# Performance work log

Hardware: AMD Instinct MI355X
Metric: run time of the kernel (lower is better)

## Reference

```python
import jax, jax.numpy as jnp
import numpy as np

EPS = 1e-5  # torch InstanceNorm2d default eps


def setup_inputs() -> dict:
    key = jax.random.key(0)
    k1, k2, k3, k4 = jax.random.split(key, 4)
    B, C, H, W = 32, 256, 64, 64
    S = 16
    x = jax.random.normal(k1, (B, C, H, W), dtype=jnp.float32)
    style_id = jax.random.randint(k2, (B,), 0, S, dtype=jnp.int64)
    gamma = jax.random.normal(k3, (S, C), dtype=jnp.float32)
    beta = jax.random.normal(k4, (S, C), dtype=jnp.float32)
    return {"x": x, "style_id": style_id, "gamma": gamma, "beta": beta}


def reference(x, style_id, gamma, beta):
    # Per-sample, per-channel instance norm over spatial dims (biased var),
    # with style-indexed affine params (torch InstanceNorm2d, affine=True).
    mean = jnp.mean(x, axis=(2, 3), keepdims=True)          # [B,C,1,1]
    var = jnp.mean(jnp.square(x - mean), axis=(2, 3), keepdims=True)
    x_hat = (x - mean) * jax.lax.rsqrt(var + EPS)
    g = gamma[style_id][:, :, None, None]                   # [B,C,1,1]
    b = beta[style_id][:, :, None, None]
    return x_hat * g + b
```

## Files before the change

kernel.cpp:

```cpp
#include <hip/hip_runtime.h>


#define HW   4096
#define NC   256
#define NTHR 256

typedef float vfloat4 __attribute__((ext_vector_type(4)));

__global__ __launch_bounds__(NTHR) void cin2d_kernel(
    const float* __restrict__ x,
    const int* __restrict__ style_id,
    const float* __restrict__ gamma,
    const float* __restrict__ beta,
    float* __restrict__ out)
{
    const int wave = threadIdx.x >> 6;
    const int lane = threadIdx.x & 63;
    const int inst = (blockIdx.x << 2) + wave;
    const int b = inst >> 8;
    const int c = inst & (NC - 1);

    const vfloat4* xp = (const vfloat4*)(x + (size_t)inst * HW) + lane;

    vfloat4 d[16];
#pragma unroll
    for (int i = 0; i < 16; ++i) d[i] = __builtin_nontemporal_load(xp + i * 64);

#pragma unroll
    for (int i = 0; i < 16; ++i) asm volatile("" : "+v"(d[i]));

    const int sid = style_id[b];
    const float g  = gamma[sid * NC + c];
    const float be = beta[sid * NC + c];

    float s0 = 0.f, s1 = 0.f, s2 = 0.f, s3 = 0.f;
    float q0 = 0.f, q1 = 0.f, q2 = 0.f, q3 = 0.f;
#pragma unroll
    for (int i = 0; i < 16; ++i) {
        s0 += d[i][0];  q0 = fmaf(d[i][0], d[i][0], q0);
        s1 += d[i][1];  q1 = fmaf(d[i][1], d[i][1], q1);
        s2 += d[i][2];  q2 = fmaf(d[i][2], d[i][2], q2);
        s3 += d[i][3];  q3 = fmaf(d[i][3], d[i][3], q3);
    }
    float s = (s0 + s1) + (s2 + s3);
    float q = (q0 + q1) + (q2 + q3);

#pragma unroll
    for (int off = 1; off < 64; off <<= 1) {
        s += __shfl_xor(s, off, 64);
        q += __shfl_xor(q, off, 64);
    }

    const float inv_n = 1.0f / (float)HW;
    const float mean = s * inv_n;
    float var = fmaf(-mean, mean, q * inv_n);
    var = var < 0.0f ? 0.0f : var;
    const float rstd = rsqrtf(var + 1e-5f);

    const float scale = g * rstd;
    const float shift = fmaf(-mean, scale, be);

    vfloat4* op = (vfloat4*)(out + (size_t)inst * HW) + lane;
#pragma unroll
    for (int i = 0; i < 16; ++i) {
        vfloat4 w;
#pragma unroll
        for (int j = 0; j < 4; ++j) w[j] = fmaf(d[i][j], scale, shift);
        op[i * 64] = w;
    }
}

extern "C" void kernel_launch(void* const* d_in, const int* in_sizes, int n_in,
                              void* d_out, int out_size, void* d_ws, size_t ws_size,
                              hipStream_t stream) {
    const float* x     = (const float*)d_in[0];
    const int*   sid   = (const int*)d_in[1];
    const float* gamma = (const float*)d_in[2];
    const float* beta  = (const float*)d_in[3];
    float* out = (float*)d_out;

    const int B = 32, C = 256;
    dim3 grid((B * C) / 4), block(NTHR);
    hipLaunchKernelGGL(cin2d_kernel, grid, block, 0, stream,
                       x, sid, gamma, beta, out);
}
```

Baseline: 228.8 us.

## Split instance norm into separate stats and apply kernels via workspace

Replaces the single fused kernel, which held each 16 KB instance in registers, with two launches. The first computes per-instance scale and shift into a workspace buffer and the second re-reads x to apply them. This frees register pressure so more waves can stay resident. In exchange x is read twice (about 128 MB extra traffic, some possibly served by the large cache) and a second launch is added.

```diff
diff --git a/kernel.cpp b/kernel.cpp
--- a/kernel.cpp
+++ b/kernel.cpp
@@ -7,12 +7,12 @@
 
 typedef float vfloat4 __attribute__((ext_vector_type(4)));
 
-__global__ __launch_bounds__(NTHR) void cin2d_kernel(
+__global__ __launch_bounds__(NTHR) void cin2d_stats(
     const float* __restrict__ x,
     const int* __restrict__ style_id,
     const float* __restrict__ gamma,
     const float* __restrict__ beta,
-    float* __restrict__ out)
+    float2* __restrict__ ss)
 {
     const int wave = threadIdx.x >> 6;
     const int lane = threadIdx.x & 63;
@@ -22,25 +22,15 @@
 
     const vfloat4* xp = (const vfloat4*)(x + (size_t)inst * HW) + lane;
 
-    vfloat4 d[16];
-#pragma unroll
-    for (int i = 0; i < 16; ++i) d[i] = __builtin_nontemporal_load(xp + i * 64);
-
-#pragma unroll
-    for (int i = 0; i < 16; ++i) asm volatile("" : "+v"(d[i]));
-
-    const int sid = style_id[b];
-    const float g  = gamma[sid * NC + c];
-    const float be = beta[sid * NC + c];
-
     float s0 = 0.f, s1 = 0.f, s2 = 0.f, s3 = 0.f;
     float q0 = 0.f, q1 = 0.f, q2 = 0.f, q3 = 0.f;
 #pragma unroll
     for (int i = 0; i < 16; ++i) {
-        s0 += d[i][0];  q0 = fmaf(d[i][0], d[i][0], q0);
-        s1 += d[i][1];  q1 = fmaf(d[i][1], d[i][1], q1);
-        s2 += d[i][2];  q2 = fmaf(d[i][2], d[i][2], q2);
-        s3 += d[i][3];  q3 = fmaf(d[i][3], d[i][3], q3);
+        const vfloat4 d = xp[i * 64];
+        s0 += d[0];  q0 = fmaf(d[0], d[0], q0);
+        s1 += d[1];  q1 = fmaf(d[1], d[1], q1);
+        s2 += d[2];  q2 = fmaf(d[2], d[2], q2);
+        s3 += d[3];  q3 = fmaf(d[3], d[3], q3);
     }
     float s = (s0 + s1) + (s2 + s3);
     float q = (q0 + q1) + (q2 + q3);
@@ -51,21 +41,43 @@
         q += __shfl_xor(q, off, 64);
     }
 
-    const float inv_n = 1.0f / (float)HW;
-    const float mean = s * inv_n;
-    float var = fmaf(-mean, mean, q * inv_n);
-    var = var < 0.0f ? 0.0f : var;
-    const float rstd = rsqrtf(var + 1e-5f);
+    if (lane == 0) {
+        const float inv_n = 1.0f / (float)HW;
+        const float mean = s * inv_n;
+        float var = fmaf(-mean, mean, q * inv_n);
+        var = var < 0.0f ? 0.0f : var;
+        const float rstd = rsqrtf(var + 1e-5f);
 
-    const float scale = g * rstd;
-    const float shift = fmaf(-mean, scale, be);
+        const int sid = style_id[b];
+        const float g  = gamma[sid * NC + c];
+        const float be = beta[sid * NC + c];
 
-    vfloat4* op = (vfloat4*)(out + (size_t)inst * HW) + lane;
+        const float scale = g * rstd;
+        const float shift = fmaf(-mean, scale, be);
+        ss[inst] = make_float2(scale, shift);
+    }
+}
+
+__global__ __launch_bounds__(NTHR) void cin2d_apply(
+    const float* __restrict__ x,
+    const float2* __restrict__ ss,
+    float* __restrict__ out)
+{
+    const int wave = threadIdx.x >> 6;
+    const int lane = threadIdx.x & 63;
+    const int inst = (blockIdx.x << 2) + wave;
+
+    const float2 p = ss[inst];
+
+    const vfloat4* xp = (const vfloat4*)(x   + (size_t)inst * HW) + lane;
+    vfloat4*       op = (vfloat4*)      (out + (size_t)inst * HW) + lane;
+
 #pragma unroll
     for (int i = 0; i < 16; ++i) {
+        const vfloat4 d = __builtin_nontemporal_load(xp + i * 64);
         vfloat4 w;
 #pragma unroll
-        for (int j = 0; j < 4; ++j) w[j] = fmaf(d[i][j], scale, shift);
+        for (int j = 0; j < 4; ++j) w[j] = fmaf(d[j], p.x, p.y);
         op[i * 64] = w;
     }
 }
@@ -78,9 +90,13 @@
     const float* gamma = (const float*)d_in[2];
     const float* beta  = (const float*)d_in[3];
     float* out = (float*)d_out;
+    float2* ss = (float2*)d_ws;
 
     const int B = 32, C = 256;
     dim3 grid((B * C) / 4), block(NTHR);
-    hipLaunchKernelGGL(cin2d_kernel, grid, block, 0, stream,
-                       x, sid, gamma, beta, out);
+
+    hipLaunchKernelGGL(cin2d_stats, grid, block, 0, stream,
+                       x, sid, gamma, beta, ss);
+    hipLaunchKernelGGL(cin2d_apply, grid, block, 0, stream,
+                       x, ss, out);
 }
```

Result: slower. 264.7 us (+15.7%).
